# Kernel tuning notes

Hardware: AMD Instinct MI355X
Metric: run time of the kernel (lower is better)

Reference implementation:

```python
import jax, jax.numpy as jnp
import numpy as np

B, S, D, H = 2, 2048, 512, 8
HD = D // H
MASK_VALUE = -1000000000.0


def setup_inputs() -> dict:
    key = jax.random.key(0)
    ks = jax.random.split(key, 12)
    scale = 1.0 / np.sqrt(D)
    return {
        "queries": jax.random.normal(ks[0], (B, S, D), dtype=jnp.float32),
        "keys": jax.random.normal(ks[1], (B, S, D), dtype=jnp.float32),
        "values": jax.random.normal(ks[2], (B, S, D), dtype=jnp.float32),
        "attn_gate": jax.random.normal(ks[3], (B, S, S, H), dtype=jnp.float32),  # [B,k,q,H]
        "attn_mask": jax.random.randint(ks[4], (B, 1, S, S), 0, 2, dtype=jnp.int32),
        "Wq": jax.random.normal(ks[5], (D, D), dtype=jnp.float32) * scale,
        "bq": jnp.zeros((D,), dtype=jnp.float32),
        "Wk": jax.random.normal(ks[6], (D, D), dtype=jnp.float32) * scale,
        "bk": jnp.zeros((D,), dtype=jnp.float32),
        "Wv": jax.random.normal(ks[7], (D, D), dtype=jnp.float32) * scale,
        "bv": jnp.zeros((D,), dtype=jnp.float32),
    }


def _split_heads(x):
    # [B, S, D] -> [B, H, S, HD]
    b, s, _ = x.shape
    return x.reshape(b, s, H, HD).transpose(0, 2, 1, 3)


def reference(queries, keys, values, attn_gate, attn_mask, Wq, bq, Wk, bk, Wv, bv):
    Q = _split_heads(queries @ Wq.T + bq)  # [B,H,q,hd]
    K = _split_heads(keys @ Wk.T + bk)     # [B,H,k,hd]
    V = _split_heads(values @ Wv.T + bv)   # [B,H,k,hd]

    scores = jnp.einsum("bhqd,bhkd->bhqk", Q, K) / jnp.sqrt(jnp.float32(HD))
    scores = scores + attn_gate.transpose(0, 3, 2, 1)  # gate [B,k,q,H] -> [B,H,q,k]
    scores = jnp.where(attn_mask == 0, MASK_VALUE, scores)
    A = jax.nn.softmax(scores, axis=-1)

    out = jnp.einsum("bhqk,bhkd->bhqd", A, V)  # [B,H,q,hd]
    b, _, q, _ = out.shape
    return out.transpose(0, 2, 1, 3).reshape(b, q, H * HD)
```

## Files before the change

kernel.cpp:

```cpp
#include <hip/hip_runtime.h>
#include <hip/hip_bf16.h>

#define B_  2
#define S_  2048
#define D_  512
#define H_  8
#define HD_ 64
#define WSN 2097152

typedef __attribute__((ext_vector_type(8))) short short8v;
typedef __attribute__((ext_vector_type(4))) float f32x4;

union U8 { ushort s[8]; uint4 v; };

__device__ __forceinline__ ushort f2bf(float x) {
    union { float f; unsigned u; } c; c.f = x;
    unsigned r = c.u + 0x7fffu + ((c.u >> 16) & 1u);
    return (ushort)(r >> 16);
}
__device__ __forceinline__ float bf2f(ushort b) {
    union { unsigned u; float f; } c; c.u = ((unsigned)b) << 16;
    return c.f;
}
__device__ __forceinline__ unsigned shflu(unsigned v, int src) {
    return (unsigned)__shfl((int)v, src, 64);
}

#define MFMA(a, b, c) __builtin_amdgcn_mfma_f32_16x16x32_bf16((a), (b), (c), 0, 0, 0)

#define PM 128
#define PN 64
#define PK 32

__global__ __launch_bounds__(256, 3)
void proj_kernel(const float* __restrict__ Xq, const float* __restrict__ Xk,
                 const float* __restrict__ Xv,
                 const float* __restrict__ Wq, const float* __restrict__ bq,
                 const float* __restrict__ Wk, const float* __restrict__ bk,
                 const float* __restrict__ Wv, const float* __restrict__ bv,
                 ushort* __restrict__ ws)
{
    const int which = blockIdx.z;
    const float* X    = which == 0 ? Xq : (which == 1 ? Xk : Xv);
    const float* W    = which == 0 ? Wq : (which == 1 ? Wk : Wv);
    const float* bias = which == 0 ? bq : (which == 1 ? bk : bv);
    ushort* outh = ws + (size_t)which * 2 * WSN;
    ushort* outl = outh + WSN;

    __shared__ __align__(16) char smem[33792];
    ushort (*Ah)[40]  = (ushort(*)[40])(smem);
    ushort (*Al)[40]  = (ushort(*)[40])(smem + 10240);
    ushort (*Bh)[40]  = (ushort(*)[40])(smem + 20480);
    ushort (*Bl)[40]  = (ushort(*)[40])(smem + 25600);
    float  (*VT)[132] = (float(*)[132])(smem);

    const int t = threadIdx.x;
    const int lane = t & 63, wid = t >> 6;
    const int g = lane >> 4, ql = lane & 15;
    const int wm = wid >> 1, wn = wid & 1;
    const int m0 = blockIdx.x * PM, n0 = blockIdx.y * PN;

    const int arow = t >> 1, ahalf = (t & 1) * 16;
    const int brow = t >> 2, bcol = (t & 3) * 8;

    f32x4 acc[4][2];
    #pragma unroll
    for (int i = 0; i < 4; ++i)
        #pragma unroll
        for (int j = 0; j < 2; ++j) acc[i][j] = (f32x4)(0.0f);

    for (int k0 = 0; k0 < D_; k0 += PK) {
        {
            const float* xp = &X[(size_t)(m0 + arow) * D_ + k0 + ahalf];
            float av[16];
            #pragma unroll
            for (int i = 0; i < 4; ++i) {
                float4 f = *(const float4*)&xp[i * 4];
                av[i*4+0] = f.x; av[i*4+1] = f.y; av[i*4+2] = f.z; av[i*4+3] = f.w;
            }
            #pragma unroll
            for (int hh = 0; hh < 2; ++hh) {
                U8 uh, ul;
                #pragma unroll
                for (int i = 0; i < 8; ++i) {
                    float v = av[hh*8 + i];
                    ushort hb = f2bf(v);
                    uh.s[i] = hb; ul.s[i] = f2bf(v - bf2f(hb));
                }
                *(uint4*)&Ah[arow][ahalf + hh*8] = uh.v;
                *(uint4*)&Al[arow][ahalf + hh*8] = ul.v;
            }
            const float* wp = &W[(size_t)(n0 + brow) * D_ + k0 + bcol];
            float4 f0 = *(const float4*)&wp[0], f1 = *(const float4*)&wp[4];
            float bw[8] = {f0.x, f0.y, f0.z, f0.w, f1.x, f1.y, f1.z, f1.w};
            U8 uh, ul;
            #pragma unroll
            for (int i = 0; i < 8; ++i) {
                ushort hb = f2bf(bw[i]);
                uh.s[i] = hb; ul.s[i] = f2bf(bw[i] - bf2f(hb));
            }
            *(uint4*)&Bh[brow][bcol] = uh.v;
            *(uint4*)&Bl[brow][bcol] = ul.v;
        }
        __syncthreads();
        short8v afh[4], afl[4], bfh[2], bfl[2];
        #pragma unroll
        for (int mf = 0; mf < 4; ++mf) {
            afh[mf] = *(const short8v*)&Ah[wm*64 + mf*16 + ql][g*8];
            afl[mf] = *(const short8v*)&Al[wm*64 + mf*16 + ql][g*8];
        }
        #pragma unroll
        for (int nf = 0; nf < 2; ++nf) {
            bfh[nf] = *(const short8v*)&Bh[wn*32 + nf*16 + ql][g*8];
            bfl[nf] = *(const short8v*)&Bl[wn*32 + nf*16 + ql][g*8];
        }
        #pragma unroll
        for (int mf = 0; mf < 4; ++mf)
            #pragma unroll
            for (int nf = 0; nf < 2; ++nf) {
                acc[mf][nf] = MFMA(afh[mf], bfh[nf], acc[mf][nf]);
                acc[mf][nf] = MFMA(afl[mf], bfh[nf], acc[mf][nf]);
                acc[mf][nf] = MFMA(afh[mf], bfl[nf], acc[mf][nf]);
            }
        __syncthreads();
    }

    float bias2[2];
    #pragma unroll
    for (int nf = 0; nf < 2; ++nf) bias2[nf] = bias[n0 + wn*32 + nf*16 + ql];

    if (which < 2) {
        #pragma unroll
        for (int mf = 0; mf < 4; ++mf)
            #pragma unroll
            for (int nf = 0; nf < 2; ++nf)
                #pragma unroll
                for (int r = 0; r < 4; ++r) {
                    int m = m0 + wm*64 + mf*16 + g*4 + r;
                    int s = m & (S_ - 1), bb = m >> 11;
                    int n = n0 + wn*32 + nf*16 + ql;
                    float v = acc[mf][nf][r] + bias2[nf];
                    ushort hb = f2bf(v), lb = f2bf(v - bf2f(hb));
                    size_t idx = ((size_t)(bb * H_ + (n >> 6)) * S_ + s) * HD_ + (n & 63);
                    outh[idx] = hb; outl[idx] = lb;
                }
    } else {
        #pragma unroll
        for (int mf = 0; mf < 4; ++mf)
            #pragma unroll
            for (int nf = 0; nf < 2; ++nf)
                #pragma unroll
                for (int r = 0; r < 4; ++r)
                    VT[wn*32 + nf*16 + ql][wm*64 + mf*16 + g*4 + r] =
                        acc[mf][nf][r] + bias2[nf];
        __syncthreads();
        const int row = t >> 2, seg = (t & 3) * 32;
        const int h = n0 >> 6, bb = m0 >> 11, s0 = m0 & (S_ - 1);
        ushort* oh = outh + ((size_t)(bb * H_ + h) * HD_ + row) * S_ + s0 + seg;
        ushort* ol = outl + ((size_t)(bb * H_ + h) * HD_ + row) * S_ + s0 + seg;
        #pragma unroll
        for (int c0 = 0; c0 < 32; c0 += 8) {
            U8 uh, ul;
            #pragma unroll
            for (int i = 0; i < 8; ++i) {
                float v = VT[row][seg + c0 + i];
                ushort hb = f2bf(v);
                uh.s[i] = hb; ul.s[i] = f2bf(v - bf2f(hb));
            }
            *(uint4*)&oh[c0] = uh.v;
            *(uint4*)&ol[c0] = ul.v;
        }
    }
}

__global__ __launch_bounds__(256, 2)
void attn_kernel(const ushort* __restrict__ ws,
                 const float* __restrict__ gate,
                 const int*   __restrict__ mask,
                 float* __restrict__ out)
{
    const ushort* Qh  = ws;
    const ushort* Qlo = ws + (size_t)WSN;
    const ushort* Kh  = ws + (size_t)2 * WSN;
    const ushort* Klo = ws + (size_t)3 * WSN;
    const ushort* Vth = ws + (size_t)4 * WSN;
    const ushort* Vtl = ws + (size_t)5 * WSN;

    __shared__ ushort VhL[64][72], VlL[64][72];

    const int bid = blockIdx.x;
    const int h = bid >> 6, b = (bid >> 5) & 1, qt = bid & 31;
    const int q0 = qt * 64;

    const int t = threadIdx.x, lane = t & 63, wid = t >> 6;
    const int g = lane >> 4, ql = lane & 15;
    const int qg = q0 + wid * 16 + ql;

    const size_t bh = (size_t)(b * H_ + h);
    const ushort* Kbh = Kh  + bh * S_ * HD_;
    const ushort* Kbl = Klo + bh * S_ * HD_;
    const ushort* Vbh = Vth + bh * HD_ * S_;
    const ushort* Vbl = Vtl + bh * HD_ * S_;
    const float*  gb  = gate + (size_t)b * S_ * S_ * H_ + (size_t)qg * H_ + h;
    const int*    mb  = mask + ((size_t)b * S_ + qg) * S_;

    short8v qfh[2], qfl[2];
    {
        const ushort* qr = Qh  + (bh * S_ + qg) * HD_;
        const ushort* qrl = Qlo + (bh * S_ + qg) * HD_;
        #pragma unroll
        for (int c2 = 0; c2 < 2; ++c2) {
            qfh[c2] = *(const short8v*)&qr[c2*32 + g*8];
            qfl[c2] = *(const short8v*)&qrl[c2*32 + g*8];
        }
    }

    f32x4 accO[4];
    #pragma unroll
    for (int i = 0; i < 4; ++i) accO[i] = (f32x4)(0.0f);
    float lpart = 0.0f;

    const int srcA = ql + ((g & 1) << 5);
    const int srcB = srcA + 16;

    for (int kt = 0; kt < S_ / 64; ++kt) {
        const int k00 = kt * 64;
        __syncthreads();
        int4 mv[4]; float gv[4][4];
        #pragma unroll
        for (int kf = 0; kf < 4; ++kf)
            mv[kf] = *(const int4*)&mb[k00 + kf*16 + g*4];
        #pragma unroll
        for (int kf = 0; kf < 4; ++kf)
            #pragma unroll
            for (int r = 0; r < 4; ++r)
                gv[kf][r] = gb[(size_t)(k00 + kf*16 + g*4 + r) * (S_ * H_)];
        #pragma unroll
        for (int i = 0; i < 2; ++i) {
            int ch = t + i * 256;
            int r = ch >> 3, c = (ch & 7) * 8;
            *(uint4*)&VhL[r][c] = *(const uint4*)&Vbh[(size_t)r * S_ + k00 + c];
            *(uint4*)&VlL[r][c] = *(const uint4*)&Vbl[(size_t)r * S_ + k00 + c];
        }
        __syncthreads();

        f32x4 accS[4];
        #pragma unroll
        for (int kf = 0; kf < 4; ++kf) accS[kf] = (f32x4)(0.0f);
        #pragma unroll
        for (int kf = 0; kf < 4; ++kf) {
            const ushort* krh = Kbh + (size_t)(k00 + kf*16 + ql) * HD_;
            const ushort* krl = Kbl + (size_t)(k00 + kf*16 + ql) * HD_;
            short8v kh0 = *(const short8v*)&krh[g*8];
            short8v kh1 = *(const short8v*)&krh[32 + g*8];
            short8v kl0 = *(const short8v*)&krl[g*8];
            short8v kl1 = *(const short8v*)&krl[32 + g*8];
            f32x4 a = accS[kf];
            a = MFMA(kh0, qfh[0], a); a = MFMA(kh1, qfh[1], a);
            a = MFMA(kl0, qfh[0], a); a = MFMA(kl1, qfh[1], a);
            a = MFMA(kh0, qfl[0], a); a = MFMA(kh1, qfl[1], a);
            accS[kf] = a;
        }

        unsigned phw[4][2], plw[4][2];
        #pragma unroll
        for (int kf = 0; kf < 4; ++kf) {
            float p[4];
            #pragma unroll
            for (int r = 0; r < 4; ++r) {
                float s = fmaf(accS[kf][r], 0.125f, gv[kf][r]);
                const int mm = (r == 0) ? mv[kf].x : (r == 1) ? mv[kf].y
                             : (r == 2) ? mv[kf].z : mv[kf].w;
                p[r] = mm ? __expf(s) : 0.0f;
                lpart += p[r];
            }
            ushort h0 = f2bf(p[0]), h1 = f2bf(p[1]), h2 = f2bf(p[2]), h3 = f2bf(p[3]);
            phw[kf][0] = ((unsigned)h1 << 16) | h0;
            phw[kf][1] = ((unsigned)h3 << 16) | h2;
            ushort l0 = f2bf(p[0] - bf2f(h0)), l1 = f2bf(p[1] - bf2f(h1));
            ushort l2 = f2bf(p[2] - bf2f(h2)), l3 = f2bf(p[3] - bf2f(h3));
            plw[kf][0] = ((unsigned)l1 << 16) | l0;
            plw[kf][1] = ((unsigned)l3 << 16) | l2;
        }

        short8v pah[2], pal[2];
        #pragma unroll
        for (int cc = 0; cc < 2; ++cc) {
            union { unsigned u[4]; short8v v; } Uh, Ul;
            #pragma unroll
            for (int w = 0; w < 2; ++w) {
                unsigned a0 = shflu(phw[2*cc][w], srcA);
                unsigned a1 = shflu(phw[2*cc + 1][w], srcA);
                Uh.u[w] = (g >= 2) ? a1 : a0;
                unsigned b0 = shflu(phw[2*cc][w], srcB);
                unsigned b1 = shflu(phw[2*cc + 1][w], srcB);
                Uh.u[2 + w] = (g >= 2) ? b1 : b0;
                unsigned c0 = shflu(plw[2*cc][w], srcA);
                unsigned c1 = shflu(plw[2*cc + 1][w], srcA);
                Ul.u[w] = (g >= 2) ? c1 : c0;
                unsigned d0 = shflu(plw[2*cc][w], srcB);
                unsigned d1 = shflu(plw[2*cc + 1][w], srcB);
                Ul.u[2 + w] = (g >= 2) ? d1 : d0;
            }
            pah[cc] = Uh.v; pal[cc] = Ul.v;
        }

        #pragma unroll
        for (int nf = 0; nf < 4; ++nf) {
            f32x4 a = accO[nf];
            #pragma unroll
            for (int cc = 0; cc < 2; ++cc) {
                short8v vh = *(const short8v*)&VhL[nf*16 + ql][cc*32 + g*8];
                short8v vl = *(const short8v*)&VlL[nf*16 + ql][cc*32 + g*8];
                a = MFMA(pah[cc], vh, a);
                a = MFMA(pal[cc], vh, a);
                a = MFMA(pah[cc], vl, a);
            }
            accO[nf] = a;
        }
    }

    lpart += __shfl_xor(lpart, 16, 64);
    lpart += __shfl_xor(lpart, 32, 64);
    float lrow[4];
    #pragma unroll
    for (int r = 0; r < 4; ++r) lrow[r] = __shfl(lpart, g*4 + r, 64);

    #pragma unroll
    for (int nf = 0; nf < 4; ++nf)
        #pragma unroll
        for (int r = 0; r < 4; ++r) {
            int qq = q0 + wid*16 + g*4 + r;
            out[((size_t)b * S_ + qq) * D_ + h * HD_ + nf*16 + ql] =
                accO[nf][r] / lrow[r];
        }
}

extern "C" void kernel_launch(void* const* d_in, const int* in_sizes, int n_in,
                              void* d_out, int out_size, void* d_ws, size_t ws_size,
                              hipStream_t stream)
{
    const float* queries = (const float*)d_in[0];
    const float* keys    = (const float*)d_in[1];
    const float* values  = (const float*)d_in[2];
    const float* gate    = (const float*)d_in[3];
    const int*   mask    = (const int*)  d_in[4];
    const float* Wq      = (const float*)d_in[5];
    const float* bq      = (const float*)d_in[6];
    const float* Wk      = (const float*)d_in[7];
    const float* bk      = (const float*)d_in[8];
    const float* Wv      = (const float*)d_in[9];
    const float* bv      = (const float*)d_in[10];

    ushort* ws = (ushort*)d_ws;
    float* outp = (float*)d_out;

    proj_kernel<<<dim3(4096 / PM, D_ / PN, 3), 256, 0, stream>>>(
        queries, keys, values, Wq, bq, Wk, bk, Wv, bv, ws);

    attn_kernel<<<dim3(B_ * H_ * (S_ / 64)), 256, 0, stream>>>(
        ws, gate, mask, outp);
}
```

Baseline: 659.3 us.

## Pre-transpose gate+mask to fp16, split-K attention with combine, LDS DMA loads

Adds a gate_prep pass that transposes the strided [B,k,q,H] gate into a per-head fp16 [bh,k,q] layout and folds the mask in as a large negative fp16 value, so the attention loop reads coalesced 2-byte values and no longer loads the mask. Inputs and weights are converted to hi/lo bf16 in separate kernels, and the projection uses global_load_lds with XOR-swizzled LDS tiles. The Q scale is folded into the projection. Attention is split four ways over keys for more blocks and occupancy, and a combine kernel merges the partials. This adds an extra pass over the large gate tensor and extra partial-output traffic. Because the softmax subtracts no max, fp16 gate precision and overflow are a risk.

```diff
diff --git a/kernel.cpp b/kernel.cpp
--- a/kernel.cpp
+++ b/kernel.cpp
@@ -1,17 +1,16 @@
 #include <hip/hip_runtime.h>
-#include <hip/hip_bf16.h>
 
 #define B_  2
 #define S_  2048
 #define D_  512
 #define H_  8
 #define HD_ 64
-#define WSN 2097152
 
 typedef __attribute__((ext_vector_type(8))) short short8v;
 typedef __attribute__((ext_vector_type(4))) float f32x4;
 
 union U8 { ushort s[8]; uint4 v; };
+union Hu { ushort u; _Float16 h; };
 
 __device__ __forceinline__ ushort f2bf(float x) {
     union { float f; unsigned u; } c; c.f = x;
@@ -25,43 +24,103 @@
 __device__ __forceinline__ unsigned shflu(unsigned v, int src) {
     return (unsigned)__shfl((int)v, src, 64);
 }
+__device__ __forceinline__ void gl2lds(const void* g, void* l) {
+    auto g1 = (const __attribute__((address_space(1))) char*)(uintptr_t)g;
+    auto l3 = (__attribute__((address_space(3))) char*)(uint32_t)(uintptr_t)l;
+    __builtin_amdgcn_global_load_lds(g1, l3, 16, 0, 0);
+}
 
 #define MFMA(a, b, c) __builtin_amdgcn_mfma_f32_16x16x32_bf16((a), (b), (c), 0, 0, 0)
 
-#define PM 128
-#define PN 64
-#define PK 32
+#define OFF_QH  67108864ull
+#define OFF_QL  69206016ull
+#define OFF_KH  71303168ull
+#define OFF_KL  73400320ull
+#define OFF_VTH 75497472ull
+#define OFF_VTL 77594624ull
+#define OFF_XH  79691776ull
+#define OFF_XL  85983232ull
+#define OFF_WH  92274688ull
+#define OFF_WL  93061120ull
+#define PARTO_BYTE 159383552ull
+
+__global__ __launch_bounds__(256)
+void gate_prep(const float* __restrict__ gate, const int* __restrict__ mask,
+               ushort* __restrict__ gT)
+{
+    const int b = blockIdx.z, k0 = blockIdx.x * 64, q0 = blockIdx.y * 64;
+    const int t = threadIdx.x;
+    const int qb = (t & 7) * 8;
+    #pragma unroll
+    for (int p = 0; p < 2; ++p) {
+        const int k = p * 32 + (t >> 3);
+        const float* gp = gate + (((size_t)b * S_ + k0 + k) * S_ + q0 + qb) * H_;
+        const int*   mp = mask + ((size_t)b * S_ + q0 + qb) * S_ + k0 + k;
+        ushort oh[8][8];
+        #pragma unroll
+        for (int j = 0; j < 8; ++j) {
+            float4 f0 = *(const float4*)(gp + (size_t)j * 8);
+            float4 f1 = *(const float4*)(gp + (size_t)j * 8 + 4);
+            int m = mp[(size_t)j * S_];
+            float vals[8] = {f0.x, f0.y, f0.z, f0.w, f1.x, f1.y, f1.z, f1.w};
+            #pragma unroll
+            for (int hh = 0; hh < 8; ++hh) {
+                Hu c; c.h = (_Float16)vals[hh];
+                oh[hh][j] = m ? c.u : (ushort)0xFB53;
+            }
+        }
+        #pragma unroll
+        for (int hh = 0; hh < 8; ++hh) {
+            U8 u;
+            #pragma unroll
+            for (int j = 0; j < 8; ++j) u.s[j] = oh[hh][j];
+            *(uint4*)&gT[((size_t)(b * 8 + hh) * S_ + k0 + k) * S_ + q0 + qb] = u.v;
+        }
+    }
+}
+
+__global__ __launch_bounds__(256)
+void cvt_kernel(const float* __restrict__ s0, const float* __restrict__ s1,
+                const float* __restrict__ s2, ushort* __restrict__ dh,
+                ushort* __restrict__ dl, int per8)
+{
+    const int which = blockIdx.y;
+    const float* s = which == 0 ? s0 : (which == 1 ? s1 : s2);
+    const size_t base = (size_t)which * per8 * 8;
+    const size_t idx = (size_t)blockIdx.x * 256 + threadIdx.x;
+    float4 f0 = *((const float4*)s + idx * 2);
+    float4 f1 = *((const float4*)s + idx * 2 + 1);
+    float v[8] = {f0.x, f0.y, f0.z, f0.w, f1.x, f1.y, f1.z, f1.w};
+    U8 uh, ul;
+    #pragma unroll
+    for (int i = 0; i < 8; ++i) {
+        ushort hb = f2bf(v[i]);
+        uh.s[i] = hb; ul.s[i] = f2bf(v[i] - bf2f(hb));
+    }
+    *(uint4*)&dh[base + idx * 8] = uh.v;
+    *(uint4*)&dl[base + idx * 8] = ul.v;
+}
 
 __global__ __launch_bounds__(256, 3)
-void proj_kernel(const float* __restrict__ Xq, const float* __restrict__ Xk,
-                 const float* __restrict__ Xv,
-                 const float* __restrict__ Wq, const float* __restrict__ bq,
-                 const float* __restrict__ Wk, const float* __restrict__ bk,
-                 const float* __restrict__ Wv, const float* __restrict__ bv,
-                 ushort* __restrict__ ws)
+void proj_kernel(const float* __restrict__ bq, const float* __restrict__ bk,
+                 const float* __restrict__ bv, ushort* __restrict__ ws16)
 {
     const int which = blockIdx.z;
-    const float* X    = which == 0 ? Xq : (which == 1 ? Xk : Xv);
-    const float* W    = which == 0 ? Wq : (which == 1 ? Wk : Wv);
+    const int h = blockIdx.y;
+    const int m0 = blockIdx.x * 128;
     const float* bias = which == 0 ? bq : (which == 1 ? bk : bv);
-    ushort* outh = ws + (size_t)which * 2 * WSN;
-    ushort* outl = outh + WSN;
-
-    __shared__ __align__(16) char smem[33792];
-    ushort (*Ah)[40]  = (ushort(*)[40])(smem);
-    ushort (*Al)[40]  = (ushort(*)[40])(smem + 10240);
-    ushort (*Bh)[40]  = (ushort(*)[40])(smem + 20480);
-    ushort (*Bl)[40]  = (ushort(*)[40])(smem + 25600);
-    float  (*VT)[132] = (float(*)[132])(smem);
-
-    const int t = threadIdx.x;
-    const int lane = t & 63, wid = t >> 6;
+
+    const ushort* xh = ws16 + OFF_XH + (size_t)which * 2097152;
+    const ushort* xl = ws16 + OFF_XL + (size_t)which * 2097152;
+    const ushort* wh = ws16 + OFF_WH + (size_t)which * 262144;
+    const ushort* wl = ws16 + OFF_WL + (size_t)which * 262144;
+
+    __shared__ __align__(16) ushort plds[24576];
+
+    const int t = threadIdx.x, lane = t & 63, wid = t >> 6;
     const int g = lane >> 4, ql = lane & 15;
     const int wm = wid >> 1, wn = wid & 1;
-    const int m0 = blockIdx.x * PM, n0 = blockIdx.y * PN;
-
-    const int arow = t >> 1, ahalf = (t & 1) * 16;
-    const int brow = t >> 2, bcol = (t & 3) * 8;
+    const int n0 = h * 64;
 
     f32x4 acc[4][2];
     #pragma unroll
@@ -69,95 +128,89 @@
         #pragma unroll
         for (int j = 0; j < 2; ++j) acc[i][j] = (f32x4)(0.0f);
 
-    for (int k0 = 0; k0 < D_; k0 += PK) {
-        {
-            const float* xp = &X[(size_t)(m0 + arow) * D_ + k0 + ahalf];
-            float av[16];
-            #pragma unroll
-            for (int i = 0; i < 4; ++i) {
-                float4 f = *(const float4*)&xp[i * 4];
-                av[i*4+0] = f.x; av[i*4+1] = f.y; av[i*4+2] = f.z; av[i*4+3] = f.w;
-            }
-            #pragma unroll
-            for (int hh = 0; hh < 2; ++hh) {
-                U8 uh, ul;
+    for (int k0 = 0; k0 < D_; k0 += 64) {
+        #pragma unroll
+        for (int c = 0; c < 4; ++c) {
+            int ch = c * 256 + t;
+            int row = ch >> 3, cb = ch & 7;
+            size_t so = (size_t)(m0 + row) * 512 + k0 + ((cb ^ (row & 7)) * 8);
+            gl2lds(xh + so, (char*)plds + c * 4096 + wid * 1024);
+            gl2lds(xl + so, (char*)plds + 16384 + c * 4096 + wid * 1024);
+        }
+        #pragma unroll
+        for (int c = 0; c < 2; ++c) {
+            int ch = c * 256 + t;
+            int row = ch >> 3, cb = ch & 7;
+            size_t so = (size_t)(n0 + row) * 512 + k0 + ((cb ^ (row & 7)) * 8);
+            gl2lds(wh + so, (char*)plds + 32768 + c * 4096 + wid * 1024);
+            gl2lds(wl + so, (char*)plds + 40960 + c * 4096 + wid * 1024);
+        }
+        __syncthreads();
+        #pragma unroll
+        for (int ks = 0; ks < 2; ++ks) {
+            short8v ah[4], al[4], bh2[2], bl2[2];
+            #pragma unroll
+            for (int mf = 0; mf < 4; ++mf) {
+                int r = wm * 64 + mf * 16 + ql;
+                int cb = ((ks * 4 + g) ^ (r & 7)) * 8;
+                ah[mf] = *(const short8v*)&plds[r * 64 + cb];
+                al[mf] = *(const short8v*)&plds[8192 + r * 64 + cb];
+            }
+            #pragma unroll
+            for (int nf = 0; nf < 2; ++nf) {
+                int n = wn * 32 + nf * 16 + ql;
+                int cb = ((ks * 4 + g) ^ (n & 7)) * 8;
+                bh2[nf] = *(const short8v*)&plds[16384 + n * 64 + cb];
+                bl2[nf] = *(const short8v*)&plds[20480 + n * 64 + cb];
+            }
+            #pragma unroll
+            for (int mf = 0; mf < 4; ++mf)
                 #pragma unroll
-                for (int i = 0; i < 8; ++i) {
-                    float v = av[hh*8 + i];
-                    ushort hb = f2bf(v);
-                    uh.s[i] = hb; ul.s[i] = f2bf(v - bf2f(hb));
+                for (int nf = 0; nf < 2; ++nf) {
+                    acc[mf][nf] = MFMA(ah[mf], bh2[nf], acc[mf][nf]);
+                    acc[mf][nf] = MFMA(al[mf], bh2[nf], acc[mf][nf]);
+                    acc[mf][nf] = MFMA(ah[mf], bl2[nf], acc[mf][nf]);
                 }
-                *(uint4*)&Ah[arow][ahalf + hh*8] = uh.v;
-                *(uint4*)&Al[arow][ahalf + hh*8] = ul.v;
-            }
-            const float* wp = &W[(size_t)(n0 + brow) * D_ + k0 + bcol];
-            float4 f0 = *(const float4*)&wp[0], f1 = *(const float4*)&wp[4];
-            float bw[8] = {f0.x, f0.y, f0.z, f0.w, f1.x, f1.y, f1.z, f1.w};
-            U8 uh, ul;
-            #pragma unroll
-            for (int i = 0; i < 8; ++i) {
-                ushort hb = f2bf(bw[i]);
-                uh.s[i] = hb; ul.s[i] = f2bf(bw[i] - bf2f(hb));
-            }
-            *(uint4*)&Bh[brow][bcol] = uh.v;
-            *(uint4*)&Bl[brow][bcol] = ul.v;
         }
         __syncthreads();
-        short8v afh[4], afl[4], bfh[2], bfl[2];
-        #pragma unroll
-        for (int mf = 0; mf < 4; ++mf) {
-            afh[mf] = *(const short8v*)&Ah[wm*64 + mf*16 + ql][g*8];
-            afl[mf] = *(const short8v*)&Al[wm*64 + mf*16 + ql][g*8];
-        }
-        #pragma unroll
-        for (int nf = 0; nf < 2; ++nf) {
-            bfh[nf] = *(const short8v*)&Bh[wn*32 + nf*16 + ql][g*8];
-            bfl[nf] = *(const short8v*)&Bl[wn*32 + nf*16 + ql][g*8];
-        }
-        #pragma unroll
-        for (int mf = 0; mf < 4; ++mf)
-            #pragma unroll
-            for (int nf = 0; nf < 2; ++nf) {
-                acc[mf][nf] = MFMA(afh[mf], bfh[nf], acc[mf][nf]);
-                acc[mf][nf] = MFMA(afl[mf], bfh[nf], acc[mf][nf]);
-                acc[mf][nf] = MFMA(afh[mf], bfl[nf], acc[mf][nf]);
-            }
-        __syncthreads();
-    }
-
-    float bias2[2];
-    #pragma unroll
-    for (int nf = 0; nf < 2; ++nf) bias2[nf] = bias[n0 + wn*32 + nf*16 + ql];
+    }
+
+    const int bb = m0 >> 11, s0 = m0 & 2047;
+    float b0 = bias[n0 + wn * 32 + ql];
+    float b1 = bias[n0 + wn * 32 + 16 + ql];
 
     if (which < 2) {
+        const float scale = (which == 0) ? 0.125f : 1.0f;
+        ushort* oh = ws16 + (which == 0 ? OFF_QH : OFF_KH);
+        ushort* ol = ws16 + (which == 0 ? OFF_QL : OFF_KL);
         #pragma unroll
         for (int mf = 0; mf < 4; ++mf)
             #pragma unroll
             for (int nf = 0; nf < 2; ++nf)
                 #pragma unroll
                 for (int r = 0; r < 4; ++r) {
-                    int m = m0 + wm*64 + mf*16 + g*4 + r;
-                    int s = m & (S_ - 1), bb = m >> 11;
-                    int n = n0 + wn*32 + nf*16 + ql;
-                    float v = acc[mf][nf][r] + bias2[nf];
+                    int s = s0 + wm * 64 + mf * 16 + g * 4 + r;
+                    int n = wn * 32 + nf * 16 + ql;
+                    float v = (acc[mf][nf][r] + (nf ? b1 : b0)) * scale;
                     ushort hb = f2bf(v), lb = f2bf(v - bf2f(hb));
-                    size_t idx = ((size_t)(bb * H_ + (n >> 6)) * S_ + s) * HD_ + (n & 63);
-                    outh[idx] = hb; outl[idx] = lb;
+                    size_t idx = ((size_t)(bb * 8 + h) * S_ + s) * 64 + n;
+                    oh[idx] = hb; ol[idx] = lb;
                 }
     } else {
+        float (*VT)[132] = (float(*)[132])plds;
         #pragma unroll
         for (int mf = 0; mf < 4; ++mf)
             #pragma unroll
             for (int nf = 0; nf < 2; ++nf)
                 #pragma unroll
                 for (int r = 0; r < 4; ++r)
-                    VT[wn*32 + nf*16 + ql][wm*64 + mf*16 + g*4 + r] =
-                        acc[mf][nf][r] + bias2[nf];
+                    VT[wn * 32 + nf * 16 + ql][wm * 64 + mf * 16 + g * 4 + r] =
+                        acc[mf][nf][r] + (nf ? b1 : b0);
         __syncthreads();
         const int row = t >> 2, seg = (t & 3) * 32;
-        const int h = n0 >> 6, bb = m0 >> 11, s0 = m0 & (S_ - 1);
-        ushort* oh = outh + ((size_t)(bb * H_ + h) * HD_ + row) * S_ + s0 + seg;
-        ushort* ol = outl + ((size_t)(bb * H_ + h) * HD_ + row) * S_ + s0 + seg;
+        ushort* oh = ws16 + OFF_VTH;
+        ushort* ol = ws16 + OFF_VTL;
+        size_t ob = ((size_t)(bb * 8 + h) * 64 + row) * S_ + s0 + seg;
         #pragma unroll
         for (int c0 = 0; c0 < 32; c0 += 8) {
             U8 uh, ul;
@@ -167,52 +220,39 @@
                 ushort hb = f2bf(v);
                 uh.s[i] = hb; ul.s[i] = f2bf(v - bf2f(hb));
             }
-            *(uint4*)&oh[c0] = uh.v;
-            *(uint4*)&ol[c0] = ul.v;
-        }
-    }
-}
-
-__global__ __launch_bounds__(256, 2)
-void attn_kernel(const ushort* __restrict__ ws,
-                 const float* __restrict__ gate,
-                 const int*   __restrict__ mask,
-                 float* __restrict__ out)
-{
-    const ushort* Qh  = ws;
-    const ushort* Qlo = ws + (size_t)WSN;
-    const ushort* Kh  = ws + (size_t)2 * WSN;
-    const ushort* Klo = ws + (size_t)3 * WSN;
-    const ushort* Vth = ws + (size_t)4 * WSN;
-    const ushort* Vtl = ws + (size_t)5 * WSN;
-
-    __shared__ ushort VhL[64][72], VlL[64][72];
-
-    const int bid = blockIdx.x;
-    const int h = bid >> 6, b = (bid >> 5) & 1, qt = bid & 31;
-    const int q0 = qt * 64;
+            *(uint4*)&oh[ob + c0] = uh.v;
+            *(uint4*)&ol[ob + c0] = ul.v;
+        }
+    }
+}
+
+__global__ __launch_bounds__(256, 4)
+void attn_kernel(const ushort* __restrict__ ws16,
+                 float* __restrict__ partO, float* __restrict__ partl)
+{
+    __shared__ __align__(16) ushort vlds[8192];
+
+    const int orig = (blockIdx.x & 7) * 256 + (blockIdx.x >> 3);
+    const int qt = orig & 31, ks = (orig >> 5) & 3, bh = orig >> 7;
+    const int q0 = qt * 64, kbase = ks * 512;
 
     const int t = threadIdx.x, lane = t & 63, wid = t >> 6;
     const int g = lane >> 4, ql = lane & 15;
     const int qg = q0 + wid * 16 + ql;
 
-    const size_t bh = (size_t)(b * H_ + h);
-    const ushort* Kbh = Kh  + bh * S_ * HD_;
-    const ushort* Kbl = Klo + bh * S_ * HD_;
-    const ushort* Vbh = Vth + bh * HD_ * S_;
-    const ushort* Vbl = Vtl + bh * HD_ * S_;
-    const float*  gb  = gate + (size_t)b * S_ * S_ * H_ + (size_t)qg * H_ + h;
-    const int*    mb  = mask + ((size_t)b * S_ + qg) * S_;
+    const ushort* Qhp = ws16 + OFF_QH + (size_t)bh * 131072;
+    const ushort* Qlp = ws16 + OFF_QL + (size_t)bh * 131072;
+    const ushort* Khp = ws16 + OFF_KH + (size_t)bh * 131072;
+    const ushort* Klp = ws16 + OFF_KL + (size_t)bh * 131072;
+    const ushort* Vhp = ws16 + OFF_VTH + (size_t)bh * 131072;
+    const ushort* Vlp = ws16 + OFF_VTL + (size_t)bh * 131072;
+    const ushort* gb  = ws16 + (size_t)bh * S_ * S_ + qg;
 
     short8v qfh[2], qfl[2];
-    {
-        const ushort* qr = Qh  + (bh * S_ + qg) * HD_;
-        const ushort* qrl = Qlo + (bh * S_ + qg) * HD_;
-        #pragma unroll
-        for (int c2 = 0; c2 < 2; ++c2) {
-            qfh[c2] = *(const short8v*)&qr[c2*32 + g*8];
-            qfl[c2] = *(const short8v*)&qrl[c2*32 + g*8];
-        }
+    #pragma unroll
+    for (int c2 = 0; c2 < 2; ++c2) {
+        qfh[c2] = *(const short8v*)&Qhp[(size_t)qg * 64 + c2 * 32 + g * 8];
+        qfl[c2] = *(const short8v*)&Qlp[(size_t)qg * 64 + c2 * 32 + g * 8];
     }
 
     f32x4 accO[4];
@@ -223,38 +263,39 @@
     const int srcA = ql + ((g & 1) << 5);
     const int srcB = srcA + 16;
 
-    for (int kt = 0; kt < S_ / 64; ++kt) {
-        const int k00 = kt * 64;
+    for (int kt = 0; kt < 8; ++kt) {
+        const int k00 = kbase + kt * 64;
         __syncthreads();
-        int4 mv[4]; float gv[4][4];
+        #pragma unroll
+        for (int c = 0; c < 2; ++c) {
+            int ch = c * 256 + t;
+            int r = ch >> 3, cb = ch & 7;
+            size_t so = (size_t)r * S_ + k00 + ((cb ^ (r & 7)) * 8);
+            gl2lds(Vhp + so, (char*)vlds + c * 4096 + wid * 1024);
+            gl2lds(Vlp + so, (char*)vlds + 8192 + c * 4096 + wid * 1024);
+        }
+        __syncthreads();
+
+        float gv[4][4];
         #pragma unroll
         for (int kf = 0; kf < 4; ++kf)
-            mv[kf] = *(const int4*)&mb[k00 + kf*16 + g*4];
-        #pragma unroll
-        for (int kf = 0; kf < 4; ++kf)
-            #pragma unroll
-            for (int r = 0; r < 4; ++r)
-                gv[kf][r] = gb[(size_t)(k00 + kf*16 + g*4 + r) * (S_ * H_)];
-        #pragma unroll
-        for (int i = 0; i < 2; ++i) {
-            int ch = t + i * 256;
-            int r = ch >> 3, c = (ch & 7) * 8;
-            *(uint4*)&VhL[r][c] = *(const uint4*)&Vbh[(size_t)r * S_ + k00 + c];
-            *(uint4*)&VlL[r][c] = *(const uint4*)&Vbl[(size_t)r * S_ + k00 + c];
-        }
-        __syncthreads();
+            #pragma unroll
+            for (int r = 0; r < 4; ++r) {
+                Hu c; c.u = gb[(size_t)(k00 + kf * 16 + g * 4 + r) * S_];
+                gv[kf][r] = (float)c.h;
+            }
 
         f32x4 accS[4];
         #pragma unroll
         for (int kf = 0; kf < 4; ++kf) accS[kf] = (f32x4)(0.0f);
         #pragma unroll
         for (int kf = 0; kf < 4; ++kf) {
-            const ushort* krh = Kbh + (size_t)(k00 + kf*16 + ql) * HD_;
-            const ushort* krl = Kbl + (size_t)(k00 + kf*16 + ql) * HD_;
-            short8v kh0 = *(const short8v*)&krh[g*8];
-            short8v kh1 = *(const short8v*)&krh[32 + g*8];
-            short8v kl0 = *(const short8v*)&krl[g*8];
-            short8v kl1 = *(const short8v*)&krl[32 + g*8];
+            const ushort* krh = Khp + (size_t)(k00 + kf * 16 + ql) * 64;
+            const ushort* krl = Klp + (size_t)(k00 + kf * 16 + ql) * 64;
+            short8v kh0 = *(const short8v*)&krh[g * 8];
+            short8v kh1 = *(const short8v*)&krh[32 + g * 8];
+            short8v kl0 = *(const short8v*)&krl[g * 8];
+            short8v kl1 = *(const short8v*)&krl[32 + g * 8];
             f32x4 a = accS[kf];
             a = MFMA(kh0, qfh[0], a); a = MFMA(kh1, qfh[1], a);
             a = MFMA(kl0, qfh[0], a); a = MFMA(kl1, qfh[1], a);
@@ -268,10 +309,7 @@
             float p[4];
             #pragma unroll
             for (int r = 0; r < 4; ++r) {
-                float s = fmaf(accS[kf][r], 0.125f, gv[kf][r]);
-                const int mm = (r == 0) ? mv[kf].x : (r == 1) ? mv[kf].y
-                             : (r == 2) ? mv[kf].z : mv[kf].w;
-                p[r] = mm ? __expf(s) : 0.0f;
+                p[r] = __expf(accS[kf][r] + gv[kf][r]);
                 lpart += p[r];
             }
             ushort h0 = f2bf(p[0]), h1 = f2bf(p[1]), h2 = f2bf(p[2]), h3 = f2bf(p[3]);
@@ -310,8 +348,9 @@
             f32x4 a = accO[nf];
             #pragma unroll
             for (int cc = 0; cc < 2; ++cc) {
-                short8v vh = *(const short8v*)&VhL[nf*16 + ql][cc*32 + g*8];
-                short8v vl = *(const short8v*)&VlL[nf*16 + ql][cc*32 + g*8];
+                int cb = ((cc * 4 + g) ^ (ql & 7)) * 8;
+                short8v vh = *(const short8v*)&vlds[(nf * 16 + ql) * 64 + cb];
+                short8v vl = *(const short8v*)&vlds[4096 + (nf * 16 + ql) * 64 + cb];
                 a = MFMA(pah[cc], vh, a);
                 a = MFMA(pal[cc], vh, a);
                 a = MFMA(pah[cc], vl, a);
@@ -320,20 +359,51 @@
         }
     }
 
+    float* po = partO + (size_t)orig * 4096;
+    #pragma unroll
+    for (int nf = 0; nf < 4; ++nf)
+        #pragma unroll
+        for (int r = 0; r < 4; ++r)
+            po[(wid * 16 + g * 4 + r) * 64 + nf * 16 + ql] = accO[nf][r];
+
     lpart += __shfl_xor(lpart, 16, 64);
     lpart += __shfl_xor(lpart, 32, 64);
-    float lrow[4];
-    #pragma unroll
-    for (int r = 0; r < 4; ++r) lrow[r] = __shfl(lpart, g*4 + r, 64);
-
-    #pragma unroll
-    for (int nf = 0; nf < 4; ++nf)
-        #pragma unroll
-        for (int r = 0; r < 4; ++r) {
-            int qq = q0 + wid*16 + g*4 + r;
-            out[((size_t)b * S_ + qq) * D_ + h * HD_ + nf*16 + ql] =
-                accO[nf][r] / lrow[r];
-        }
+    if (lane < 16) partl[(size_t)orig * 64 + wid * 16 + lane] = lpart;
+}
+
+__global__ __launch_bounds__(256)
+void combine_kernel(const float* __restrict__ partO, const float* __restrict__ partl,
+                    float* __restrict__ out)
+{
+    const int cid = blockIdx.x;
+    const int bh = cid >> 5, qt = cid & 31;
+    const int t = threadIdx.x;
+    const int q = t >> 2, c4 = (t & 3) * 16;
+
+    float4 sum[4];
+    #pragma unroll
+    for (int i = 0; i < 4; ++i) sum[i] = make_float4(0.f, 0.f, 0.f, 0.f);
+    float l = 0.0f;
+
+    #pragma unroll
+    for (int ks = 0; ks < 4; ++ks) {
+        int p = (bh * 4 + ks) * 32 + qt;
+        const float* base = partO + (size_t)p * 4096 + q * 64 + c4;
+        #pragma unroll
+        for (int i = 0; i < 4; ++i) {
+            float4 v = *(const float4*)(base + i * 4);
+            sum[i].x += v.x; sum[i].y += v.y; sum[i].z += v.z; sum[i].w += v.w;
+        }
+        l += partl[(size_t)p * 64 + q];
+    }
+    float inv = 1.0f / l;
+    const int b = bh >> 3, h = bh & 7;
+    float* ob = out + ((size_t)b * S_ + qt * 64 + q) * D_ + h * 64 + c4;
+    #pragma unroll
+    for (int i = 0; i < 4; ++i) {
+        float4 w = make_float4(sum[i].x * inv, sum[i].y * inv, sum[i].z * inv, sum[i].w * inv);
+        *(float4*)(ob + i * 4) = w;
+    }
 }
 
 extern "C" void kernel_launch(void* const* d_in, const int* in_sizes, int n_in,
@@ -352,12 +422,17 @@
     const float* Wv      = (const float*)d_in[9];
     const float* bv      = (const float*)d_in[10];
 
-    ushort* ws = (ushort*)d_ws;
-    float* outp = (float*)d_out;
-
-    proj_kernel<<<dim3(4096 / PM, D_ / PN, 3), 256, 0, stream>>>(
-        queries, keys, values, Wq, bq, Wk, bk, Wv, bv, ws);
-
-    attn_kernel<<<dim3(B_ * H_ * (S_ / 64)), 256, 0, stream>>>(
-        ws, gate, mask, outp);
-}
+    ushort* ws16 = (ushort*)d_ws;
+    float* partO = (float*)((char*)d_ws + PARTO_BYTE);
+    float* partl = partO + 8388608;
+    float* outp  = (float*)d_out;
+
+    gate_prep<<<dim3(32, 32, 2), 256, 0, stream>>>(gate, mask, ws16);
+    cvt_kernel<<<dim3(1024, 3), 256, 0, stream>>>(
+        queries, keys, values, ws16 + OFF_XH, ws16 + OFF_XL, 262144);
+    cvt_kernel<<<dim3(128, 3), 256, 0, stream>>>(
+        Wq, Wk, Wv, ws16 + OFF_WH, ws16 + OFF_WL, 32768);
+    proj_kernel<<<dim3(32, 8, 3), 256, 0, stream>>>(bq, bk, bv, ws16);
+    attn_kernel<<<dim3(2048), 256, 0, stream>>>(ws16, partO, partl);
+    combine_kernel<<<dim3(512), 256, 0, stream>>>(partO, partl, outp);
+}
```

New measurement: 651.2 us. Within noise of the previous version (-1.2%).
